# Optimization experiments

Measured on AMD Instinct MI355X. Metric: run time of the kernel, lower is better.

Reference implementation:

```python
import jax, jax.numpy as jnp
import numpy as np

C, H, N, B, L = 1, 512, 64, 16, 2048  # n_channels, n_heads, d_kernel, batch, seq_len


def setup_inputs() -> dict:
    key = jax.random.key(0)
    k1, k2 = jax.random.split(key)
    u = jax.random.normal(k1, (B, C * H, L), dtype=jnp.float32)
    k = jax.random.normal(k2, (C, H, N), dtype=jnp.float32)
    return {"u": u, "k": k}


def _l1_normalize(x, axis):
    # torch.linalg.norm(x, ord=1, dim=axis, keepdim=True): vector 1-norm along `axis`
    return x / jnp.sum(jnp.abs(x), axis=axis, keepdims=True)


def _forward(u, k):
    c, h, n = k.shape
    bsz, d, l = u.shape  # d == c*h
    dt = u.dtype
    # Shift matrix A: A[:, :, 1:, :-1] = I  (companion-style shift)
    A = jnp.zeros((c, h, n, n), dtype=dt).at[:, :, 1:, :-1].set(jnp.eye(n - 1, dtype=dt))
    # b = e1 broadcast to (c, h, n)
    b_vec = jnp.zeros((c, h, n), dtype=dt).at[:, :, 0].set(1.0)
    # closed-loop: k_norm = L1-normalize(clamp(k, 1/16, 1)); A_cl = L1-normalize(A + b k^T)
    k_norm = _l1_normalize(jnp.clip(k, 1.0 / 16.0, 1.0), axis=2)
    BK = jnp.einsum('chi,chj->chij', b_vec, k_norm)
    M = _l1_normalize(A + BK, axis=2)

    # Krylov recurrence: f[i] = k . (M^i b), i = 0..l-1
    def step(x, _):
        f_i = jnp.einsum('chn,chn->ch', k, x)
        x_next = jnp.einsum('chij,chj->chi', M, x)
        return x_next, f_i

    _, f = jax.lax.scan(step, b_vec, None, length=l)  # f: (l, c, h)
    f = jnp.moveaxis(f, 0, -1)  # (c, h, l)

    # Causal FFT convolution of u (b, c, h, l) with filter f (c, h, l)
    n_fft = 2 * l
    uf = jnp.fft.rfft(u.reshape(bsz, c, h, l), n=n_fft)
    ff = jnp.fft.rfft(f, n=n_fft)
    y = jnp.fft.irfft(uf * ff[None], n=n_fft)[..., :l]
    return y.reshape(bsz, c * h, l)


def reference(u, k):
    return _forward(u, k)
```

## Files before the change

### kernel.cpp

```cpp
#include <hip/hip_runtime.h>


namespace {

constexpr int kH = 512;
constexpr int kL = 2048;
constexpr int kChunks = 32;
constexpr int kStride = 68;

typedef __attribute__((ext_vector_type(8))) short bf16x8;
typedef __attribute__((ext_vector_type(4))) float f32x4;

#define MFMA(A, B, C) __builtin_amdgcn_mfma_f32_16x16x32_bf16((A), (B), (C), 0, 0, 0)

__device__ inline unsigned int cvt_pk_bf16(float lo, float hi) {
  unsigned int r;
  asm("v_cvt_pk_bf16_f32 %0, %1, %2" : "=v"(r) : "v"(lo), "v"(hi));
  return r;
}

union B8U4 { bf16x8 v; unsigned int u[4]; };

__device__ inline void cvt_split8(const f32x4 a, const f32x4 b, bf16x8& fh, bf16x8& fl) {
  B8U4 H, L;
  float x[8];
  #pragma unroll
  for (int j = 0; j < 4; ++j) { x[j] = a[j]; x[4 + j] = b[j]; }
  #pragma unroll
  for (int d = 0; d < 4; ++d) {
    const float x0 = x[2 * d], x1 = x[2 * d + 1];
    const unsigned int hp = cvt_pk_bf16(x0, x1);
    const float h0 = __uint_as_float(hp << 16);
    const float h1 = __uint_as_float(hp & 0xFFFF0000u);
    H.u[d] = hp;
    L.u[d] = cvt_pk_bf16(x0 - h0, x1 - h1);
  }
  fh = H.v; fl = L.v;
}

__device__ inline void gen_frag(const float* tp, int n0, bf16x8& fh, bf16x8& fl) {
  float t[8];
  #pragma unroll
  for (int j = 0; j < 8; ++j) {
    const int n = n0 - j;
    t[j] = (n >= 0 && n < 127) ? tp[n] : 0.0f;
  }
  const f32x4 a = {t[0], t[1], t[2], t[3]};
  const f32x4 b = {t[4], t[5], t[6], t[7]};
  cvt_split8(a, b, fh, fl);
}

__global__ __launch_bounds__(64, 1)
void ssm_mfma_kernel(const float* __restrict__ u,
                     const float* __restrict__ kin,
                     float* __restrict__ y) {
  const int h    = blockIdx.x;
  const int lane = threadIdx.x;
  const int ln16 = lane & 15;
  const int quad = lane >> 4;

  __shared__ float taps[3][128];
  __shared__ float wPad[128];
  __shared__ float Abuf[64][kStride];
  __shared__ float Rbuf[16][kStride];
  __shared__ bf16x8 g2T[4][2][2][64];
  __shared__ bf16x8 g1T[4][2][2][64];

  const float kv = kin[h * 64 + lane];
  const float kc = fminf(fmaxf(kv, 0.0625f), 1.0f);
  float ks = kc;
  #pragma unroll
  for (int off = 32; off >= 1; off >>= 1) ks += __shfl_xor(ks, off);
  const float kn = kc / ks;
  const float cc = 1.0f / (1.0f + kn);
  float pp = cc;
  #pragma unroll
  for (int off = 1; off < 64; off <<= 1) {
    const float t = __shfl_up(pp, off);
    if (lane >= off) pp *= t;
  }
  float Pe = __shfl_up(pp, 1);
  if (lane == 0) Pe = 1.0f;
  const float w = (lane < 63) ? (kn * cc * Pe) : Pe;
  const float g = kv * Pe;
  float s = (lane == 0) ? 1.0f : 0.0f;
  for (int rr = 0; rr < 63; ++rr) {
    const float sv = __shfl(s, rr);
    const float cf = __shfl(w, lane - 1 - rr);
    if (lane > rr) s = fmaf(cf, sv, s);
  }
  taps[0][lane] = 0.0f;
  taps[1][lane] = 0.0f;
  const float gn = __shfl(g, lane + 1);
  taps[2][lane] = (lane < 63) ? gn : 0.0f;
  taps[2][64 + lane] = 0.0f;
  taps[0][63 + lane] = s;
  taps[1][63 + lane] = g;
  wPad[lane] = w;
  wPad[64 + lane] = 0.0f;
  __syncthreads();

  bf16x8 sH[4][2], sL[4][2], aH[4][2], aL[4][2];
  #pragma unroll
  for (int mt = 0; mt < 4; ++mt) {
    #pragma unroll
    for (int tk = 0; tk < 2; ++tk) {
      const int n0 = 16 * mt + ln16 - (32 * tk + 8 * quad) + 63;
      gen_frag(taps[0], n0, sH[mt][tk], sL[mt][tk]);
      bf16x8 fh, fl;
      gen_frag(taps[1], n0, fh, fl);
      g2T[mt][tk][0][lane] = fh;
      g2T[mt][tk][1][lane] = fl;
      gen_frag(taps[2], n0, fh, fl);
      g1T[mt][tk][0][lane] = fh;
      g1T[mt][tk][1][lane] = fl;
    }
  }

  {
    bf16x8 wh[4][2], wl[4][2];
    #pragma unroll
    for (int nt = 0; nt < 4; ++nt) {
      #pragma unroll
      for (int tk = 0; tk < 2; ++tk) {
        float t[8];
        #pragma unroll
        for (int j = 0; j < 8; ++j)
          t[j] = wPad[(8 * quad + 32 * tk + j) - (16 * nt + ln16) + 63];
        const f32x4 a = {t[0], t[1], t[2], t[3]};
        const f32x4 b = {t[4], t[5], t[6], t[7]};
        cvt_split8(a, b, wh[nt][tk], wl[nt][tk]);
      }
    }
    #pragma unroll
    for (int mt = 0; mt < 4; ++mt) {
      f32x4 accA[4];
      #pragma unroll
      for (int nt = 0; nt < 4; ++nt) accA[nt] = (f32x4){0.f, 0.f, 0.f, 0.f};
      #pragma unroll
      for (int nt = 0; nt < 4; ++nt) {
        #pragma unroll
        for (int tk = 0; tk < 2; ++tk) {
          accA[nt] = MFMA(sH[mt][tk], wh[nt][tk], accA[nt]);
          accA[nt] = MFMA(sH[mt][tk], wl[nt][tk], accA[nt]);
          accA[nt] = MFMA(sL[mt][tk], wh[nt][tk], accA[nt]);
          accA[nt] = MFMA(sL[mt][tk], wl[nt][tk], accA[nt]);
        }
      }
      #pragma unroll
      for (int nt = 0; nt < 4; ++nt) {
        #pragma unroll
        for (int r = 0; r < 4; ++r)
          Abuf[16 * mt + 4 * quad + r][16 * nt + ln16] = accA[nt][r];
      }
    }
  }
  __syncthreads();
  #pragma unroll
  for (int mt = 0; mt < 4; ++mt) {
    #pragma unroll
    for (int tk = 0; tk < 2; ++tk) {
      const int row = 16 * mt + ln16;
      const int k0 = 32 * tk + 8 * quad;
      const f32x4 a = *(const f32x4*)&Abuf[row][k0];
      const f32x4 b = *(const f32x4*)&Abuf[row][k0 + 4];
      cvt_split8(a, b, aH[mt][tk], aL[mt][tk]);
    }
  }

  bf16x8 pH[2], pL[2];
  {
    bf16x8 z;
    #pragma unroll
    for (int j = 0; j < 8; ++j) z[j] = 0;
    pH[0] = z; pH[1] = z; pL[0] = z; pL[1] = z;
  }

  const float* ub = u + ((size_t)ln16 * kH + h) * kL + 8 * quad;
  float* yp = y + ((size_t)ln16 * kH + h) * kL + 4 * quad;

  auto chunk = [&](f32x4 (&uvC)[4], int t0, int tpre) {
    bf16x8 uH[2], uL[2];
    cvt_split8(uvC[0], uvC[1], uH[0], uL[0]);
    cvt_split8(uvC[2], uvC[3], uH[1], uL[1]);
    #pragma unroll
    for (int i = 0; i < 4; ++i)
      uvC[i] = *(const f32x4*)(ub + tpre + 32 * (i >> 1) + 4 * (i & 1));

    f32x4 accR[4], accY[4];
    #pragma unroll
    for (int mt = 0; mt < 4; ++mt) {
      accR[mt] = (f32x4){0.f, 0.f, 0.f, 0.f};
      accY[mt] = (f32x4){0.f, 0.f, 0.f, 0.f};
    }
    #pragma unroll
    for (int mt = 0; mt < 4; ++mt) {
      #pragma unroll
      for (int tk = 0; tk < 2; ++tk) {
        accR[mt] = MFMA(aH[mt][tk], pH[tk], accR[mt]);
        accR[mt] = MFMA(aH[mt][tk], pL[tk], accR[mt]);
        accR[mt] = MFMA(aL[mt][tk], pH[tk], accR[mt]);
      }
      #pragma unroll
      for (int tk = 0; tk < 2; ++tk) {
        accR[mt] = MFMA(sH[mt][tk], uH[tk], accR[mt]);
        accR[mt] = MFMA(sH[mt][tk], uL[tk], accR[mt]);
        accR[mt] = MFMA(sL[mt][tk], uH[tk], accR[mt]);
      }
    }
    #pragma unroll
    for (int mt = 0; mt < 4; ++mt)
      *(f32x4*)&Rbuf[ln16][16 * mt + 4 * quad] = accR[mt];

    #pragma unroll
    for (int mt = 0; mt < 4; ++mt) {
      #pragma unroll
      for (int tk = 0; tk < 2; ++tk) {
        const bf16x8 gh = g1T[mt][tk][0][lane];
        const bf16x8 gl = g1T[mt][tk][1][lane];
        accY[mt] = MFMA(gh, pH[tk], accY[mt]);
        accY[mt] = MFMA(gh, pL[tk], accY[mt]);
        accY[mt] = MFMA(gl, pH[tk], accY[mt]);
      }
    }

    asm volatile("s_waitcnt lgkmcnt(0)" ::: "memory");
    __builtin_amdgcn_sched_barrier(0);
    #pragma unroll
    for (int tk = 0; tk < 2; ++tk) {
      const int k0 = 8 * quad + 32 * tk;
      const f32x4 ra = *(const f32x4*)&Rbuf[ln16][k0];
      const f32x4 rb = *(const f32x4*)&Rbuf[ln16][k0 + 4];
      cvt_split8(ra, rb, pH[tk], pL[tk]);
    }

    #pragma unroll
    for (int mt = 0; mt < 4; ++mt) {
      #pragma unroll
      for (int tk = 0; tk < 2; ++tk) {
        const bf16x8 gh = g2T[mt][tk][0][lane];
        const bf16x8 gl = g2T[mt][tk][1][lane];
        accY[mt] = MFMA(gh, pH[tk], accY[mt]);
        accY[mt] = MFMA(gh, pL[tk], accY[mt]);
        accY[mt] = MFMA(gl, pH[tk], accY[mt]);
      }
      *(f32x4*)(yp + t0 + 16 * mt) = accY[mt];
    }
  };

  f32x4 uvA[4], uvB[4];
  #pragma unroll
  for (int i = 0; i < 4; ++i) {
    uvA[i] = *(const f32x4*)(ub + 32 * (i >> 1) + 4 * (i & 1));
    uvB[i] = *(const f32x4*)(ub + 64 + 32 * (i >> 1) + 4 * (i & 1));
  }
  for (int m = 0; m < kChunks; m += 2) {
    const int t0 = m * 64;
    chunk(uvA, t0,      (t0 + 128 < kL) ? (t0 + 128) : 0);
    chunk(uvB, t0 + 64, (t0 + 192 < kL) ? (t0 + 192) : 0);
  }
}

}

extern "C" void kernel_launch(void* const* d_in, const int* in_sizes, int n_in,
                              void* d_out, int out_size, void* d_ws, size_t ws_size,
                              hipStream_t stream) {
  const float* u  = (const float*)d_in[0];
  const float* kk = (const float*)d_in[1];
  if (n_in >= 2 && in_sizes[0] < in_sizes[1]) {
    const float* t = u; u = kk; kk = t;
  }
  float* y = (float*)d_out;
  hipLaunchKernelGGL(ssm_mfma_kernel, dim3(kH), dim3(64), 0, stream, u, kk, y);
}
```

Before: 145.9 us.

## Split chunked SSM scan across four waves with a serial state wave and parallel output waves

Moves from one wavefront per head to four. Wave 0 runs only the serial state recurrence across 64-sample chunks, passing states through a double-buffered LDS ring. Waves 1-3 compute the input-driven chunk contributions and the outputs in a software pipeline. The setup precomputes composed operators (G2·S and G2·A + G1) with MFMA so the per-chunk output path needs fewer products. The aim is to shorten the serial critical path and overlap the u loads and output MFMAs with the recurrence, at the cost of about 120KB of LDS and a block barrier per step.

```diff
diff --git a/kernel.cpp b/kernel.cpp
--- a/kernel.cpp
+++ b/kernel.cpp
@@ -5,8 +5,6 @@
 
 constexpr int kH = 512;
 constexpr int kL = 2048;
-constexpr int kChunks = 32;
-constexpr int kStride = 68;
 
 typedef __attribute__((ext_vector_type(8))) short bf16x8;
 typedef __attribute__((ext_vector_type(4))) float f32x4;
@@ -50,123 +48,190 @@
   cvt_split8(a, b, fh, fl);
 }
 
-__global__ __launch_bounds__(64, 1)
+__device__ inline void gen_fragB(const float* tp, int base, bf16x8& fh, bf16x8& fl) {
+  float t[8];
+  #pragma unroll
+  for (int j = 0; j < 8; ++j) t[j] = tp[base + j];
+  const f32x4 a = {t[0], t[1], t[2], t[3]};
+  const f32x4 b = {t[4], t[5], t[6], t[7]};
+  cvt_split8(a, b, fh, fl);
+}
+
+
+__global__ __launch_bounds__(256, 1)
 void ssm_mfma_kernel(const float* __restrict__ u,
                      const float* __restrict__ kin,
                      float* __restrict__ y) {
   const int h    = blockIdx.x;
-  const int lane = threadIdx.x;
+  const int tid  = threadIdx.x;
+  const int wid  = tid >> 6;
+  const int lane = tid & 63;
   const int ln16 = lane & 15;
   const int quad = lane >> 4;
 
-  __shared__ float taps[3][128];
-  __shared__ float wPad[128];
-  __shared__ float Abuf[64][kStride];
-  __shared__ float Rbuf[16][kStride];
-  __shared__ bf16x8 g2T[4][2][2][64];
-  __shared__ bf16x8 g1T[4][2][2][64];
-
-  const float kv = kin[h * 64 + lane];
-  const float kc = fminf(fmaxf(kv, 0.0625f), 1.0f);
-  float ks = kc;
-  #pragma unroll
-  for (int off = 32; off >= 1; off >>= 1) ks += __shfl_xor(ks, off);
-  const float kn = kc / ks;
-  const float cc = 1.0f / (1.0f + kn);
-  float pp = cc;
-  #pragma unroll
-  for (int off = 1; off < 64; off <<= 1) {
-    const float t = __shfl_up(pp, off);
-    if (lane >= off) pp *= t;
-  }
-  float Pe = __shfl_up(pp, 1);
-  if (lane == 0) Pe = 1.0f;
-  const float w = (lane < 63) ? (kn * cc * Pe) : Pe;
-  const float g = kv * Pe;
-  float s = (lane == 0) ? 1.0f : 0.0f;
-  for (int rr = 0; rr < 63; ++rr) {
-    const float sv = __shfl(s, rr);
-    const float cf = __shfl(w, lane - 1 - rr);
-    if (lane > rr) s = fmaf(cf, sv, s);
-  }
-  taps[0][lane] = 0.0f;
-  taps[1][lane] = 0.0f;
-  const float gn = __shfl(g, lane + 1);
-  taps[2][lane] = (lane < 63) ? gn : 0.0f;
-  taps[2][64 + lane] = 0.0f;
-  taps[0][63 + lane] = s;
-  taps[1][63 + lane] = g;
-  wPad[lane] = w;
-  wPad[64 + lane] = 0.0f;
-  __syncthreads();
-
-  bf16x8 sH[4][2], sL[4][2], aH[4][2], aL[4][2];
-  #pragma unroll
-  for (int mt = 0; mt < 4; ++mt) {
+  __shared__ alignas(16) char pool[123136];
+  auto cring   = (float (*)[4][16][68]) (pool);
+  auto Astage  = (float (*)[68]) (pool);
+  auto Pstage  = (float (*)[68]) (pool + 17408);
+  auto pring   = (bf16x8 (*)[4][4][64]) (pool + 34816);
+  auto S_T     = (bf16x8 (*)[2][2][64]) (pool + 67584);
+  auto G2S_T   = (bf16x8 (*)[2][2][64]) (pool + 83968);
+  auto Gp_T    = (bf16x8 (*)[2][2][64]) (pool + 100352);
+  auto scratch = (float (*)[68]) (pool + 116736);
+  auto taps    = (float (*)[128]) (pool + 121088);
+  float* wPad  = (float*) (pool + 122624);
+
+  if (wid == 0) {
+    const float kv = kin[h * 64 + lane];
+    const float kc = fminf(fmaxf(kv, 0.0625f), 1.0f);
+    float ks = kc;
+    #pragma unroll
+    for (int off = 32; off >= 1; off >>= 1) ks += __shfl_xor(ks, off);
+    const float kn = kc / ks;
+    const float cc = 1.0f / (1.0f + kn);
+    float pp = cc;
+    #pragma unroll
+    for (int off = 1; off < 64; off <<= 1) {
+      const float t = __shfl_up(pp, off);
+      if (lane >= off) pp *= t;
+    }
+    float Pe = __shfl_up(pp, 1);
+    if (lane == 0) Pe = 1.0f;
+    const float wv = (lane < 63) ? (kn * cc * Pe) : Pe;
+    const float gv = kv * Pe;
+    float sv = (lane == 0) ? 1.0f : 0.0f;
+    for (int rr = 0; rr < 63; ++rr) {
+      const float s0 = __shfl(sv, rr);
+      const float cf = __shfl(wv, lane - 1 - rr);
+      if (lane > rr) sv = fmaf(cf, s0, sv);
+    }
+    taps[0][lane] = 0.0f;
+    taps[1][lane] = 0.0f;
+    const float gn = __shfl(gv, lane + 1);
+    taps[2][lane] = (lane < 63) ? gn : 0.0f;
+    taps[2][64 + lane] = 0.0f;
+    taps[0][63 + lane] = sv;
+    taps[1][63 + lane] = gv;
+    if (lane == 0) { taps[0][127] = 0.0f; taps[1][127] = 0.0f; }
+    wPad[lane] = wv;
+    wPad[64 + lane] = 0.0f;
+  }
+  __syncthreads();
+
+  {
+    const int mt = wid;
+    bf16x8 xh[2], xl[2], g2h[2], g2l[2];
     #pragma unroll
     for (int tk = 0; tk < 2; ++tk) {
       const int n0 = 16 * mt + ln16 - (32 * tk + 8 * quad) + 63;
-      gen_frag(taps[0], n0, sH[mt][tk], sL[mt][tk]);
+      gen_frag(taps[0], n0, xh[tk], xl[tk]);
+      gen_frag(taps[1], n0, g2h[tk], g2l[tk]);
+    }
+    #pragma unroll
+    for (int nt = 0; nt < 4; ++nt) {
+      f32x4 accA = {0.f, 0.f, 0.f, 0.f};
+      f32x4 accG = {0.f, 0.f, 0.f, 0.f};
+      #pragma unroll
+      for (int tk = 0; tk < 2; ++tk) {
+        const int base = 8 * quad + 32 * tk - (16 * nt + ln16) + 63;
+        bf16x8 bh, bl;
+        gen_fragB(wPad, base, bh, bl);
+        accA = MFMA(xh[tk], bh, accA);
+        accA = MFMA(xh[tk], bl, accA);
+        accA = MFMA(xl[tk], bh, accA);
+        accA = MFMA(xl[tk], bl, accA);
+        bf16x8 sbh, sbl;
+        gen_fragB(taps[0], base, sbh, sbl);
+        accG = MFMA(g2h[tk], sbh, accG);
+        accG = MFMA(g2h[tk], sbl, accG);
+        accG = MFMA(g2l[tk], sbh, accG);
+      }
+      #pragma unroll
+      for (int r = 0; r < 4; ++r) {
+        Astage[16 * mt + 4 * quad + r][16 * nt + ln16] = accA[r];
+        Pstage[16 * mt + 4 * quad + r][16 * nt + ln16] = accG[r];
+      }
+    }
+  }
+  __syncthreads();
+
+  {
+    const int mt = wid;
+    #pragma unroll
+    for (int tk = 0; tk < 2; ++tk) {
+      const int n0 = 16 * mt + ln16 - (32 * tk + 8 * quad) + 63;
       bf16x8 fh, fl;
-      gen_frag(taps[1], n0, fh, fl);
-      g2T[mt][tk][0][lane] = fh;
-      g2T[mt][tk][1][lane] = fl;
-      gen_frag(taps[2], n0, fh, fl);
-      g1T[mt][tk][0][lane] = fh;
-      g1T[mt][tk][1][lane] = fl;
-    }
-  }
-
-  {
-    bf16x8 wh[4][2], wl[4][2];
+      gen_frag(taps[0], n0, fh, fl);
+      S_T[mt][tk][0][lane] = fh;  S_T[mt][tk][1][lane] = fl;
+      const int row = 16 * mt + ln16, k0 = 32 * tk + 8 * quad;
+      const f32x4 a = *(const f32x4*)&Pstage[row][k0];
+      const f32x4 b = *(const f32x4*)&Pstage[row][k0 + 4];
+      cvt_split8(a, b, fh, fl);
+      G2S_T[mt][tk][0][lane] = fh;  G2S_T[mt][tk][1][lane] = fl;
+    }
+  }
+  __syncthreads();
+
+  {
+    const int mt = wid;
+    bf16x8 g2h[2], g2l[2];
+    #pragma unroll
+    for (int tk = 0; tk < 2; ++tk) {
+      const int n0 = 16 * mt + ln16 - (32 * tk + 8 * quad) + 63;
+      gen_frag(taps[1], n0, g2h[tk], g2l[tk]);
+    }
     #pragma unroll
     for (int nt = 0; nt < 4; ++nt) {
+      f32x4 acc = {0.f, 0.f, 0.f, 0.f};
       #pragma unroll
       for (int tk = 0; tk < 2; ++tk) {
         float t[8];
         #pragma unroll
         for (int j = 0; j < 8; ++j)
-          t[j] = wPad[(8 * quad + 32 * tk + j) - (16 * nt + ln16) + 63];
+          t[j] = Astage[8 * quad + 32 * tk + j][16 * nt + ln16];
         const f32x4 a = {t[0], t[1], t[2], t[3]};
         const f32x4 b = {t[4], t[5], t[6], t[7]};
-        cvt_split8(a, b, wh[nt][tk], wl[nt][tk]);
-      }
-    }
+        bf16x8 bh, bl;
+        cvt_split8(a, b, bh, bl);
+        acc = MFMA(g2h[tk], bh, acc);
+        acc = MFMA(g2h[tk], bl, acc);
+        acc = MFMA(g2l[tk], bh, acc);
+      }
+      #pragma unroll
+      for (int r = 0; r < 4; ++r) {
+        const int i = 16 * mt + 4 * quad + r, j = 16 * nt + ln16;
+        Pstage[i][j] = acc[r] + taps[2][(i - j) + 63];
+      }
+    }
+  }
+  __syncthreads();
+
+  bf16x8 aH[4][2], aL[4][2];
+  {
+    const int mt = wid;
+    #pragma unroll
+    for (int tk = 0; tk < 2; ++tk) {
+      const int row = 16 * mt + ln16, k0 = 32 * tk + 8 * quad;
+      const f32x4 a = *(const f32x4*)&Pstage[row][k0];
+      const f32x4 b = *(const f32x4*)&Pstage[row][k0 + 4];
+      bf16x8 fh, fl;
+      cvt_split8(a, b, fh, fl);
+      Gp_T[mt][tk][0][lane] = fh;  Gp_T[mt][tk][1][lane] = fl;
+    }
+  }
+  if (wid == 0) {
     #pragma unroll
     for (int mt = 0; mt < 4; ++mt) {
-      f32x4 accA[4];
-      #pragma unroll
-      for (int nt = 0; nt < 4; ++nt) accA[nt] = (f32x4){0.f, 0.f, 0.f, 0.f};
-      #pragma unroll
-      for (int nt = 0; nt < 4; ++nt) {
-        #pragma unroll
-        for (int tk = 0; tk < 2; ++tk) {
-          accA[nt] = MFMA(sH[mt][tk], wh[nt][tk], accA[nt]);
-          accA[nt] = MFMA(sH[mt][tk], wl[nt][tk], accA[nt]);
-          accA[nt] = MFMA(sL[mt][tk], wh[nt][tk], accA[nt]);
-          accA[nt] = MFMA(sL[mt][tk], wl[nt][tk], accA[nt]);
-        }
-      }
-      #pragma unroll
-      for (int nt = 0; nt < 4; ++nt) {
-        #pragma unroll
-        for (int r = 0; r < 4; ++r)
-          Abuf[16 * mt + 4 * quad + r][16 * nt + ln16] = accA[nt][r];
-      }
-    }
-  }
-  __syncthreads();
-  #pragma unroll
-  for (int mt = 0; mt < 4; ++mt) {
-    #pragma unroll
-    for (int tk = 0; tk < 2; ++tk) {
-      const int row = 16 * mt + ln16;
-      const int k0 = 32 * tk + 8 * quad;
-      const f32x4 a = *(const f32x4*)&Abuf[row][k0];
-      const f32x4 b = *(const f32x4*)&Abuf[row][k0 + 4];
-      cvt_split8(a, b, aH[mt][tk], aL[mt][tk]);
-    }
-  }
+      #pragma unroll
+      for (int tk = 0; tk < 2; ++tk) {
+        const int row = 16 * mt + ln16, k0 = 32 * tk + 8 * quad;
+        const f32x4 a = *(const f32x4*)&Astage[row][k0];
+        const f32x4 b = *(const f32x4*)&Astage[row][k0 + 4];
+        cvt_split8(a, b, aH[mt][tk], aL[mt][tk]);
+      }
+    }
+  }
+  __syncthreads();
 
   bf16x8 pH[2], pL[2];
   {
@@ -177,87 +242,132 @@
   }
 
   const float* ub = u + ((size_t)ln16 * kH + h) * kL + 8 * quad;
-  float* yp = y + ((size_t)ln16 * kH + h) * kL + 4 * quad;
-
-  auto chunk = [&](f32x4 (&uvC)[4], int t0, int tpre) {
-    bf16x8 uH[2], uL[2];
-    cvt_split8(uvC[0], uvC[1], uH[0], uL[0]);
-    cvt_split8(uvC[2], uvC[3], uH[1], uL[1]);
-    #pragma unroll
-    for (int i = 0; i < 4; ++i)
-      uvC[i] = *(const f32x4*)(ub + tpre + 32 * (i >> 1) + 4 * (i & 1));
-
-    f32x4 accR[4], accY[4];
-    #pragma unroll
-    for (int mt = 0; mt < 4; ++mt) {
-      accR[mt] = (f32x4){0.f, 0.f, 0.f, 0.f};
-      accY[mt] = (f32x4){0.f, 0.f, 0.f, 0.f};
-    }
-    #pragma unroll
-    for (int mt = 0; mt < 4; ++mt) {
-      #pragma unroll
-      for (int tk = 0; tk < 2; ++tk) {
-        accR[mt] = MFMA(aH[mt][tk], pH[tk], accR[mt]);
-        accR[mt] = MFMA(aH[mt][tk], pL[tk], accR[mt]);
-        accR[mt] = MFMA(aL[mt][tk], pH[tk], accR[mt]);
-      }
-      #pragma unroll
-      for (int tk = 0; tk < 2; ++tk) {
-        accR[mt] = MFMA(sH[mt][tk], uH[tk], accR[mt]);
-        accR[mt] = MFMA(sH[mt][tk], uL[tk], accR[mt]);
-        accR[mt] = MFMA(sL[mt][tk], uH[tk], accR[mt]);
-      }
-    }
-    #pragma unroll
-    for (int mt = 0; mt < 4; ++mt)
-      *(f32x4*)&Rbuf[ln16][16 * mt + 4 * quad] = accR[mt];
-
-    #pragma unroll
-    for (int mt = 0; mt < 4; ++mt) {
-      #pragma unroll
-      for (int tk = 0; tk < 2; ++tk) {
-        const bf16x8 gh = g1T[mt][tk][0][lane];
-        const bf16x8 gl = g1T[mt][tk][1][lane];
-        accY[mt] = MFMA(gh, pH[tk], accY[mt]);
-        accY[mt] = MFMA(gh, pL[tk], accY[mt]);
-        accY[mt] = MFMA(gl, pH[tk], accY[mt]);
-      }
-    }
-
+  float* yb = y + ((size_t)ln16 * kH + h) * kL;
+
+  f32x4 urC[4][4];
+  if (wid != 0) {
+    #pragma unroll
+    for (int cj = 0; cj < 4; ++cj)
+      #pragma unroll
+      for (int i = 0; i < 4; ++i)
+        urC[cj][i] = *(const f32x4*)(ub + 64 * cj + 32 * (i >> 1) + 4 * (i & 1));
+  }
+
+  f32x4 yuE[6], yuO[6];
+
+  auto step = [&](int s, f32x4 (&yu)[6]) {
+    if (wid == 0) {
+      if (s >= 1 && s <= 8) {
+        const int g = s - 1, gp = g & 1;
+        for (int cj = 0; cj < 4; ++cj) {
+          pring[gp][cj][0][lane] = pH[0];
+          pring[gp][cj][1][lane] = pH[1];
+          pring[gp][cj][2][lane] = pL[0];
+          pring[gp][cj][3][lane] = pL[1];
+          #pragma unroll
+          for (int mt = 0; mt < 4; ++mt) {
+            f32x4 acc = *(const f32x4*)&cring[gp][cj][ln16][16 * mt + 4 * quad];
+            #pragma unroll
+            for (int tk = 0; tk < 2; ++tk) {
+              acc = MFMA(aH[mt][tk], pH[tk], acc);
+              acc = MFMA(aH[mt][tk], pL[tk], acc);
+              acc = MFMA(aL[mt][tk], pH[tk], acc);
+            }
+            *(f32x4*)&scratch[ln16][16 * mt + 4 * quad] = acc;
+          }
+          asm volatile("s_waitcnt lgkmcnt(0)" ::: "memory");
+          __builtin_amdgcn_sched_barrier(0);
+          #pragma unroll
+          for (int tk = 0; tk < 2; ++tk) {
+            const int k0 = 8 * quad + 32 * tk;
+            const f32x4 ra = *(const f32x4*)&scratch[ln16][k0];
+            const f32x4 rb = *(const f32x4*)&scratch[ln16][k0 + 4];
+            cvt_split8(ra, rb, pH[tk], pL[tk]);
+          }
+        }
+      }
+    } else {
+      bf16x8 uH[4][2], uL[4][2];
+      if (s < 8) {
+        #pragma unroll
+        for (int cj = 0; cj < 4; ++cj) {
+          cvt_split8(urC[cj][0], urC[cj][1], uH[cj][0], uL[cj][0]);
+          cvt_split8(urC[cj][2], urC[cj][3], uH[cj][1], uL[cj][1]);
+        }
+        if (s < 7) {
+          #pragma unroll
+          for (int cj = 0; cj < 4; ++cj)
+            #pragma unroll
+            for (int i = 0; i < 4; ++i)
+              urC[cj][i] = *(const f32x4*)(ub + 64 * (4 * (s + 1) + cj) +
+                                           32 * (i >> 1) + 4 * (i & 1));
+        }
+      }
+      if (s >= 2) {
+        const int gf = s - 2;
+        #pragma unroll
+        for (int cj = 0; cj < 4; ++cj) {
+          bf16x8 pfH[2], pfL[2];
+          pfH[0] = pring[s & 1][cj][0][lane];
+          pfH[1] = pring[s & 1][cj][1][lane];
+          pfL[0] = pring[s & 1][cj][2][lane];
+          pfL[1] = pring[s & 1][cj][3][lane];
+          #pragma unroll
+          for (int mt = 0; mt < 4; ++mt) {
+            const int t = 4 * cj + mt, li = t / 3;
+            if ((t % 3) + 1 == wid) {
+              f32x4 acc = yu[li];
+              #pragma unroll
+              for (int tk = 0; tk < 2; ++tk) {
+                const bf16x8 gh = Gp_T[mt][tk][0][lane];
+                const bf16x8 gl = Gp_T[mt][tk][1][lane];
+                acc = MFMA(gh, pfH[tk], acc);
+                acc = MFMA(gh, pfL[tk], acc);
+                acc = MFMA(gl, pfH[tk], acc);
+              }
+              *(f32x4*)(yb + 64 * (4 * gf + cj) + 16 * mt + 4 * quad) = acc;
+            }
+          }
+        }
+      }
+      if (s < 8) {
+        #pragma unroll
+        for (int cj = 0; cj < 4; ++cj) {
+          #pragma unroll
+          for (int mt = 0; mt < 4; ++mt) {
+            const int t = 4 * cj + mt, li = t / 3;
+            if ((t % 3) + 1 == wid) {
+              f32x4 accC = {0.f, 0.f, 0.f, 0.f};
+              f32x4 accU = {0.f, 0.f, 0.f, 0.f};
+              #pragma unroll
+              for (int tk = 0; tk < 2; ++tk) {
+                const bf16x8 sh = S_T[mt][tk][0][lane];
+                const bf16x8 sl = S_T[mt][tk][1][lane];
+                accC = MFMA(sh, uH[cj][tk], accC);
+                accC = MFMA(sh, uL[cj][tk], accC);
+                accC = MFMA(sl, uH[cj][tk], accC);
+                const bf16x8 gh = G2S_T[mt][tk][0][lane];
+                const bf16x8 gl = G2S_T[mt][tk][1][lane];
+                accU = MFMA(gh, uH[cj][tk], accU);
+                accU = MFMA(gh, uL[cj][tk], accU);
+                accU = MFMA(gl, uH[cj][tk], accU);
+              }
+              *(f32x4*)&cring[s & 1][cj][ln16][16 * mt + 4 * quad] = accC;
+              yu[li] = accU;
+            }
+          }
+        }
+      }
+    }
     asm volatile("s_waitcnt lgkmcnt(0)" ::: "memory");
-    __builtin_amdgcn_sched_barrier(0);
-    #pragma unroll
-    for (int tk = 0; tk < 2; ++tk) {
-      const int k0 = 8 * quad + 32 * tk;
-      const f32x4 ra = *(const f32x4*)&Rbuf[ln16][k0];
-      const f32x4 rb = *(const f32x4*)&Rbuf[ln16][k0 + 4];
-      cvt_split8(ra, rb, pH[tk], pL[tk]);
-    }
-
-    #pragma unroll
-    for (int mt = 0; mt < 4; ++mt) {
-      #pragma unroll
-      for (int tk = 0; tk < 2; ++tk) {
-        const bf16x8 gh = g2T[mt][tk][0][lane];
-        const bf16x8 gl = g2T[mt][tk][1][lane];
-        accY[mt] = MFMA(gh, pH[tk], accY[mt]);
-        accY[mt] = MFMA(gh, pL[tk], accY[mt]);
-        accY[mt] = MFMA(gl, pH[tk], accY[mt]);
-      }
-      *(f32x4*)(yp + t0 + 16 * mt) = accY[mt];
-    }
+    __builtin_amdgcn_s_barrier();
+    asm volatile("" ::: "memory");
   };
 
-  f32x4 uvA[4], uvB[4];
-  #pragma unroll
-  for (int i = 0; i < 4; ++i) {
-    uvA[i] = *(const f32x4*)(ub + 32 * (i >> 1) + 4 * (i & 1));
-    uvB[i] = *(const f32x4*)(ub + 64 + 32 * (i >> 1) + 4 * (i & 1));
-  }
-  for (int m = 0; m < kChunks; m += 2) {
-    const int t0 = m * 64;
-    chunk(uvA, t0,      (t0 + 128 < kL) ? (t0 + 128) : 0);
-    chunk(uvB, t0 + 64, (t0 + 192 < kL) ? (t0 + 192) : 0);
+  #pragma unroll 1
+  for (int sb = 0; sb < 5; ++sb) {
+    step(2 * sb,     yuE);
+    step(2 * sb + 1, yuO);
   }
 }
 
@@ -271,6 +381,6 @@
   if (n_in >= 2 && in_sizes[0] < in_sizes[1]) {
     const float* t = u; u = kk; kk = t;
   }
-  float* y = (float*)d_out;
-  hipLaunchKernelGGL(ssm_mfma_kernel, dim3(kH), dim3(64), 0, stream, u, kk, y);
-}
+  float* yy = (float*)d_out;
+  hipLaunchKernelGGL(ssm_mfma_kernel, dim3(kH), dim3(256), 0, stream, u, kk, yy);
+}
```

Measured after the change: 173.9 us. +19.2%, slower.
